# Performance work log

Measured on AMD Instinct MI355X. Metric: run time of the kernel, lower is better.

The kernel has to match this reference:

```python
import jax, jax.numpy as jnp
import numpy as np

B, C, H, W = 2, 256, 100, 100
G, P = 4, 8
CG = C // G  # 64 per-group channels
EPS = 1e-5


def setup_inputs() -> dict:
    key = jax.random.key(0)
    ks = jax.random.split(key, 5)
    bev_query = jax.random.normal(ks[0], (B, C, H, W), dtype=jnp.float32)
    pts = jax.random.normal(ks[1], (B, H * W, 1, P, C), dtype=jnp.float32)
    conv_w = jax.random.normal(ks[2], (G * CG * CG, C), dtype=jnp.float32) * (1.0 / np.sqrt(C))
    conv_b = jax.random.normal(ks[3], (G * CG * CG,), dtype=jnp.float32) * 0.02
    ln_g = jnp.ones((CG,), dtype=jnp.float32)
    ln_b = jnp.zeros((CG,), dtype=jnp.float32)
    proj_w = jax.random.normal(ks[4], (CG, CG * P), dtype=jnp.float32) * (1.0 / np.sqrt(CG * P))
    proj_b = jnp.zeros((CG,), dtype=jnp.float32)
    return {"bev_query": bev_query, "pts": pts, "conv_w": conv_w, "conv_b": conv_b,
            "ln_g": ln_g, "ln_b": ln_b, "proj_w": proj_w, "proj_b": proj_b}


def reference(bev_query, pts, conv_w, conv_b, ln_g, ln_b, proj_w, proj_b):
    b, c, h, w = bev_query.shape
    q = h * w
    # pts: b q 1 p c -> b q p c
    pts = jnp.squeeze(pts, axis=2)
    # 1x1 conv parameter generator: b c h w -> b (g c1 c2) h w
    param = jnp.einsum('bchw,oc->bohw', bev_query, conv_w) + conv_b[None, :, None, None]
    # 'b (g c1 c2) h w -> (b g) (h w) c1 c2'
    param = param.reshape(b, G, CG, CG, q).transpose(0, 1, 4, 2, 3).reshape(b * G, q, CG, CG)
    # 'b q p (g c) -> (b g) q p c'
    pts_g = pts.reshape(b, q, P, G, CG).transpose(0, 3, 1, 2, 4).reshape(b * G, q, P, CG)
    # batched per-pixel matmul: (bg,q,p,c1) @ (bg,q,c1,c2) -> (bg,q,p,c2)
    mixed = jnp.matmul(pts_g, param)
    # LayerNorm over last dim + ReLU
    mu = jnp.mean(mixed, axis=-1, keepdims=True)
    var = jnp.var(mixed, axis=-1, keepdims=True)
    normed = (mixed - mu) * jax.lax.rsqrt(var + EPS) * ln_g + ln_b
    act = jax.nn.relu(normed)
    # 'b q p c -> b q (p c)' then linear
    flat = act.reshape(b * G, q, P * CG)
    out = jnp.einsum('bqi,oi->bqo', flat, proj_w) + proj_b
    # '(b g) (h w) c -> b (g c) h w'
    out = out.reshape(b, G, q, CG).transpose(0, 1, 3, 2).reshape(b, G * CG, h, w)
    return out
```

## Files before the change

### kernel.cpp

```cpp
#include <hip/hip_runtime.h>
#include <hip/hip_bf16.h>
#include <stdint.h>

#define QTOT 10000
#define MPAD 10240
#define CDIM 256
#define ODIM 16384
#define RTOT 20096

using f32x4  = __attribute__((ext_vector_type(4))) float;
using bf16x8 = __attribute__((ext_vector_type(8))) short;

#define GLOAD_LDS(gp, lp) __builtin_amdgcn_global_load_lds(                     \
    (const __attribute__((address_space(1))) unsigned int*)(gp),                \
    (__attribute__((address_space(3))) unsigned int*)(lp), 16, 0, 0)

static __device__ __forceinline__ short f2bs(float x) {
  __hip_bfloat16 h = __float2bfloat16(x);
  return *(short*)&h;
}

__global__ void cvt_f32_bf16(const float* __restrict__ s, __hip_bfloat16* __restrict__ d, int n) {
  for (int i = blockIdx.x * blockDim.x + threadIdx.x; i < n; i += gridDim.x * blockDim.x)
    d[i] = __float2bfloat16(s[i]);
}

__global__ void cvt_permute_cw(const float* __restrict__ s, __hip_bfloat16* __restrict__ d, int n) {
  for (int i = blockIdx.x * blockDim.x + threadIdx.x; i < n; i += gridDim.x * blockDim.x) {
    int rn = i >> 8, c = i & 255;
    int ro = (rn & ~4095) | ((rn & 63) << 6) | ((rn >> 6) & 63);
    d[i] = __float2bfloat16(s[ro * 256 + c]);
  }
}

__global__ __launch_bounds__(256) void transpose_bev(const float* __restrict__ bev,
                                                     __hip_bfloat16* __restrict__ bevT) {
  __shared__ float tl[32][33];
  int tx = threadIdx.x, ty = threadIdx.y;
  int q0 = blockIdx.x * 32, c0 = blockIdx.y * 32, b = blockIdx.z;
#pragma unroll
  for (int i = 0; i < 4; ++i) {
    int c = c0 + ty + i * 8, q = q0 + tx;
    tl[ty + i * 8][tx] = (q < QTOT) ? bev[((size_t)b * CDIM + c) * QTOT + q] : 0.0f;
  }
  __syncthreads();
#pragma unroll
  for (int i = 0; i < 4; ++i) {
    int q = q0 + ty + i * 8, c = c0 + tx;
    bevT[((size_t)b * MPAD + q) * CDIM + c] = __float2bfloat16(tl[tx][ty + i * 8]);
  }
}

__global__ __launch_bounds__(256) void gemm_param(const __hip_bfloat16* __restrict__ A,
                                                  const __hip_bfloat16* __restrict__ Bw,
                                                  const float* __restrict__ convb,
                                                  __hip_bfloat16* __restrict__ P) {
  __shared__ __align__(16) unsigned char lsA[2][16384];
  __shared__ __align__(16) unsigned char lsB[2][16384];
  int t = threadIdx.x, lane = t & 63, w = t >> 6;
  int bm = blockIdx.x, bn = blockIdx.y;
  int wm = (w >> 1) * 64, wn = (w & 1) * 64;
  int srow = lane >> 3;
  int kbs  = ((lane & 7) ^ srow) * 8;
  const __hip_bfloat16* pA = A  + (size_t)(bm * 128 + w * 32 + srow) * CDIM + kbs;
  const __hip_bfloat16* pB = Bw + (size_t)(bn * 128 + w * 32 + srow) * CDIM + kbs;
  f32x4 acc[4][4] = {};

#define STAGE_P(buf, kt) do {                                                   \
    _Pragma("unroll")                                                           \
    for (int i = 0; i < 4; ++i) {                                               \
      GLOAD_LDS(pA + (size_t)i * 8 * CDIM + (kt), lsA[buf] + (w * 4 + i) * 1024); \
      GLOAD_LDS(pB + (size_t)i * 8 * CDIM + (kt), lsB[buf] + (w * 4 + i) * 1024); \
    } } while (0)

  STAGE_P(0, 0);
  asm volatile("s_waitcnt vmcnt(0)" ::: "memory");
  __builtin_amdgcn_s_barrier();
#pragma unroll
  for (int kt = 0; kt < 4; ++kt) {
    const int cur = kt & 1;
    if (kt < 3) STAGE_P(cur ^ 1, (kt + 1) * 64);
    __builtin_amdgcn_sched_barrier(0);
#pragma unroll
    for (int kk = 0; kk < 2; ++kk) {
      int kb = kk * 64 + ((lane >> 4) << 4);
      bf16x8 af[4], bfr[4];
#pragma unroll
      for (int mi = 0; mi < 4; ++mi) {
        int row = wm + mi * 16 + (lane & 15);
        af[mi] = *(const bf16x8*)(lsA[cur] + ((row * 128 + kb) ^ ((row & 7) << 4)));
      }
#pragma unroll
      for (int ni = 0; ni < 4; ++ni) {
        int row = wn + ni * 16 + (lane & 15);
        bfr[ni] = *(const bf16x8*)(lsB[cur] + ((row * 128 + kb) ^ ((row & 7) << 4)));
      }
#pragma unroll
      for (int mi = 0; mi < 4; ++mi)
#pragma unroll
        for (int ni = 0; ni < 4; ++ni)
          acc[mi][ni] = __builtin_amdgcn_mfma_f32_16x16x32_bf16(af[mi], bfr[ni], acc[mi][ni], 0, 0, 0);
    }
    __builtin_amdgcn_sched_barrier(0);
    if (kt < 3) asm volatile("s_waitcnt vmcnt(0)" ::: "memory");
    __builtin_amdgcn_s_barrier();
    __builtin_amdgcn_sched_barrier(0);
  }
#pragma unroll
  for (int ni = 0; ni < 4; ++ni) {
    int col = bn * 128 + wn + ni * 16 + (lane & 15);
    int o_old = (col & ~4095) | ((col & 63) << 6) | ((col >> 6) & 63);
    float cb = convb[o_old];
#pragma unroll
    for (int mi = 0; mi < 4; ++mi) {
      int rb = bm * 128 + wm + mi * 16 + ((lane >> 4) << 2);
#pragma unroll
      for (int r = 0; r < 4; ++r)
        P[(size_t)(rb + r) * ODIM + col] = __float2bfloat16(acc[mi][ni][r] + cb);
    }
  }
#undef STAGE_P
}

__global__ __launch_bounds__(256) void mix_mfma(const __hip_bfloat16* __restrict__ P,
                                                const float* __restrict__ pts,
                                                const float* __restrict__ lng,
                                                const float* __restrict__ lnb,
                                                __hip_bfloat16* __restrict__ act,
                                                int b, int q0) {
  __shared__ __align__(16) float ptsl[8 * 264];
  int t = threadIdx.x, lane = t & 63, g = t >> 6;
  int row = blockIdx.x;
  size_t rq = (size_t)b * QTOT + q0 + row;
  {
    const float4* ps = (const float4*)(pts + rq * 2048);
#pragma unroll
    for (int i = 0; i < 2; ++i) {
      int v = i * 256 + t;
      float4 val = ps[v];
      int p = v >> 6, c = (v & 63) * 4;
      *(float4*)(ptsl + p * 264 + c) = val;
    }
  }
  __syncthreads();
  int l15 = lane & 15, hi = lane >> 4;
  bf16x8 bfr[2];
#pragma unroll
  for (int kk = 0; kk < 2; ++kk) {
    bf16x8 v = {};
    if (l15 < 8) {
      const float* src = ptsl + l15 * 264 + g * 64 + kk * 32 + hi * 8;
#pragma unroll
      for (int j = 0; j < 8; ++j) v[j] = f2bs(src[j]);
    }
    bfr[kk] = v;
  }
  const __hip_bfloat16* Ap = P + (size_t)row * ODIM + g * 4096;
  f32x4 acc[4] = {};
#pragma unroll
  for (int kk = 0; kk < 2; ++kk)
#pragma unroll
    for (int mi = 0; mi < 4; ++mi) {
      bf16x8 a = *(const bf16x8*)(Ap + (size_t)(mi * 16 + l15) * 64 + kk * 32 + hi * 8);
      acc[mi] = __builtin_amdgcn_mfma_f32_16x16x32_bf16(a, bfr[kk], acc[mi], 0, 0, 0);
    }
  float s = 0.f, ss = 0.f;
#pragma unroll
  for (int mi = 0; mi < 4; ++mi)
#pragma unroll
    for (int r = 0; r < 4; ++r) { float v = acc[mi][r]; s += v; ss = fmaf(v, v, ss); }
  s += __shfl_xor(s, 16);  ss += __shfl_xor(ss, 16);
  s += __shfl_xor(s, 32);  ss += __shfl_xor(ss, 32);
  float mu  = s * 0.015625f;
  float var = ss * 0.015625f - mu * mu;
  float rs  = rsqrtf(var + 1e-5f);
  if (l15 < 8) {
    short* ab = (short*)act + ((size_t)g * RTOT + rq) * 512 + l15 * 64;
#pragma unroll
    for (int mi = 0; mi < 4; ++mi) {
      int c2 = mi * 16 + hi * 4;
      float4 gg = *(const float4*)(lng + c2);
      float4 bb = *(const float4*)(lnb + c2);
      short4 o;
      o.x = f2bs(fmaxf(0.f, (acc[mi][0] - mu) * rs * gg.x + bb.x));
      o.y = f2bs(fmaxf(0.f, (acc[mi][1] - mu) * rs * gg.y + bb.y));
      o.z = f2bs(fmaxf(0.f, (acc[mi][2] - mu) * rs * gg.z + bb.z));
      o.w = f2bs(fmaxf(0.f, (acc[mi][3] - mu) * rs * gg.w + bb.w));
      *(short4*)(ab + c2) = o;
    }
  }
}

__global__ __launch_bounds__(256) void gemm_proj(const __hip_bfloat16* __restrict__ act,
                                                 const __hip_bfloat16* __restrict__ Bp,
                                                 const float* __restrict__ projb,
                                                 float* __restrict__ outT) {
  __shared__ __align__(16) unsigned char lsA[2][16384];
  __shared__ __align__(16) unsigned char lsB[2][8192];
  int t = threadIdx.x, lane = t & 63, w = t >> 6;
  int bm = blockIdx.x, g = blockIdx.y;
  int wm = (w >> 1) * 64, wn = (w & 1) * 32;
  int srow = lane >> 3;
  int kbs  = ((lane & 7) ^ srow) * 8;
  const __hip_bfloat16* A  = act + (size_t)g * RTOT * 512;
  const __hip_bfloat16* pA = A  + (size_t)(bm * 128 + w * 32 + srow) * 512 + kbs;
  const __hip_bfloat16* pB = Bp + (size_t)(w * 16 + srow) * 512 + kbs;
  f32x4 acc[4][2] = {};

#define STAGE_Q(buf, kt) do {                                                   \
    _Pragma("unroll")                                                           \
    for (int i = 0; i < 4; ++i)                                                 \
      GLOAD_LDS(pA + (size_t)i * 8 * 512 + (kt), lsA[buf] + (w * 4 + i) * 1024); \
    _Pragma("unroll")                                                           \
    for (int j = 0; j < 2; ++j)                                                 \
      GLOAD_LDS(pB + (size_t)j * 8 * 512 + (kt), lsB[buf] + (w * 2 + j) * 1024); \
    } while (0)

  STAGE_Q(0, 0);
  asm volatile("s_waitcnt vmcnt(0)" ::: "memory");
  __builtin_amdgcn_s_barrier();
#pragma unroll
  for (int kt = 0; kt < 8; ++kt) {
    const int cur = kt & 1;
    if (kt < 7) STAGE_Q(cur ^ 1, (kt + 1) * 64);
    __builtin_amdgcn_sched_barrier(0);
#pragma unroll
    for (int kk = 0; kk < 2; ++kk) {
      int kb = kk * 64 + ((lane >> 4) << 4);
      bf16x8 af[4], bfr[2];
#pragma unroll
      for (int mi = 0; mi < 4; ++mi) {
        int row = wm + mi * 16 + (lane & 15);
        af[mi] = *(const bf16x8*)(lsA[cur] + ((row * 128 + kb) ^ ((row & 7) << 4)));
      }
#pragma unroll
      for (int ni = 0; ni < 2; ++ni) {
        int row = wn + ni * 16 + (lane & 15);
        bfr[ni] = *(const bf16x8*)(lsB[cur] + ((row * 128 + kb) ^ ((row & 7) << 4)));
      }
#pragma unroll
      for (int mi = 0; mi < 4; ++mi)
#pragma unroll
        for (int ni = 0; ni < 2; ++ni)
          acc[mi][ni] = __builtin_amdgcn_mfma_f32_16x16x32_bf16(af[mi], bfr[ni], acc[mi][ni], 0, 0, 0);
    }
    __builtin_amdgcn_sched_barrier(0);
    if (kt < 7) asm volatile("s_waitcnt vmcnt(0)" ::: "memory");
    __builtin_amdgcn_s_barrier();
    __builtin_amdgcn_sched_barrier(0);
  }
#pragma unroll
  for (int ni = 0; ni < 2; ++ni) {
    int o = wn + ni * 16 + (lane & 15);
    float pb = projb[o];
#pragma unroll
    for (int mi = 0; mi < 4; ++mi) {
      int rb = bm * 128 + wm + mi * 16 + ((lane >> 4) << 2);
#pragma unroll
      for (int r = 0; r < 4; ++r) {
        int rg = rb + r;
        if (rg < 2 * QTOT)
          outT[(size_t)rg * CDIM + g * 64 + o] = acc[mi][ni][r] + pb;
      }
    }
  }
#undef STAGE_Q
}

__global__ __launch_bounds__(256) void transpose_out(const float* __restrict__ outT,
                                                     float* __restrict__ out) {
  __shared__ float tl[32][33];
  int tx = threadIdx.x, ty = threadIdx.y;
  int q0 = blockIdx.x * 32, c0 = blockIdx.y * 32, b = blockIdx.z;
#pragma unroll
  for (int i = 0; i < 4; ++i) {
    int q = q0 + ty + i * 8, c = c0 + tx;
    tl[ty + i * 8][tx] = (q < QTOT) ? outT[((size_t)b * QTOT + q) * CDIM + c] : 0.0f;
  }
  __syncthreads();
#pragma unroll
  for (int i = 0; i < 4; ++i) {
    int c = c0 + ty + i * 8, q = q0 + tx;
    if (q < QTOT) out[((size_t)b * CDIM + c) * QTOT + q] = tl[tx][ty + i * 8];
  }
}

extern "C" void kernel_launch(void* const* d_in, const int* in_sizes, int n_in,
                              void* d_out, int out_size, void* d_ws, size_t ws_size,
                              hipStream_t stream) {
  const float* bev = (const float*)d_in[0];
  const float* pts = (const float*)d_in[1];
  const float* cw  = (const float*)d_in[2];
  const float* cb  = (const float*)d_in[3];
  const float* lng = (const float*)d_in[4];
  const float* lnb = (const float*)d_in[5];
  const float* pw  = (const float*)d_in[6];
  const float* pb  = (const float*)d_in[7];
  float* out = (float*)d_out;

  char* ws = (char*)d_ws;
  size_t off = 0;
  auto carve = [&](size_t bytes) -> char* {
    char* p = ws + off;
    off += (bytes + 255) & ~(size_t)255;
    return p;
  };
  __hip_bfloat16* cw_bf = (__hip_bfloat16*)carve((size_t)ODIM * CDIM * 2);
  __hip_bfloat16* bevT  = (__hip_bfloat16*)carve((size_t)2 * MPAD * CDIM * 2);
  __hip_bfloat16* pw_bf = (__hip_bfloat16*)carve((size_t)64 * 512 * 2);
  float* outT           = (float*)carve((size_t)2 * QTOT * CDIM * 4);
  __hip_bfloat16* act   = (__hip_bfloat16*)carve((size_t)4 * RTOT * 512 * 2);
  size_t fixed = off;

  int CH = 128;
  const int ladder[4] = {2560, 1280, 640, 128};
  for (int i = 0; i < 4; ++i) {
    size_t need = fixed + (((size_t)ladder[i] * ODIM * 2 + 255) & ~(size_t)255);
    if (need <= ws_size) { CH = ladder[i]; break; }
  }
  __hip_bfloat16* param = (__hip_bfloat16*)carve((size_t)CH * ODIM * 2);

  cvt_permute_cw<<<4096, 256, 0, stream>>>(cw, cw_bf, ODIM * CDIM);
  cvt_f32_bf16<<<128, 256, 0, stream>>>(pw, pw_bf, 64 * 512);
  transpose_bev<<<dim3(MPAD / 32, CDIM / 32, 2), dim3(32, 8), 0, stream>>>(bev, bevT);

  int nchunks = (QTOT + CH - 1) / CH;
  for (int b = 0; b < 2; ++b) {
    for (int c = 0; c < nchunks; ++c) {
      int q0 = c * CH;
      int nvalid = QTOT - q0;
      if (nvalid > CH) nvalid = CH;
      const __hip_bfloat16* Ab = bevT + ((size_t)b * MPAD + q0) * CDIM;
      gemm_param<<<dim3(CH / 128, ODIM / 128), 256, 0, stream>>>(Ab, cw_bf, cb, param);
      mix_mfma<<<dim3(nvalid), 256, 0, stream>>>(param, pts, lng, lnb, act, b, q0);
    }
  }
  gemm_proj<<<dim3(RTOT / 128, 4), 256, 0, stream>>>(act, pw_bf, pb, outT);
  transpose_out<<<dim3((QTOT + 31) / 32, CDIM / 32, 2), dim3(32, 8), 0, stream>>>(outT, out);
}
```

Baseline: 537.2 us.

## Enlarge param GEMM tile to 256x256 with 512 threads and block swizzle

Grows the parameter-generation GEMM block tile from 128x128 to 256x256, using 8 waves each computing a 128x64 sub-tile and doubling the LDS stage buffers. Block indices are remapped in groups of 8 to spread neighbouring tiles, which is meant to improve cache locality. The goal is more reuse of each staged A/B tile per global load. In mix_mfma the LDS staging of pts and the block barrier are replaced by direct float4 global loads. The chunk ladder drops the 1280/640 options, so small workspaces fall back to 256-row chunks. Risks are higher register and LDS pressure lowering occupancy, and fewer blocks per launch.

Measured after the change: 580.3 us. 8.0% more time.

```diff
diff --git a/kernel.cpp b/kernel.cpp
--- a/kernel.cpp
+++ b/kernel.cpp
@@ -51,20 +51,25 @@
   }
 }
 
-__global__ __launch_bounds__(256) void gemm_param(const __hip_bfloat16* __restrict__ A,
-                                                  const __hip_bfloat16* __restrict__ Bw,
-                                                  const float* __restrict__ convb,
-                                                  __hip_bfloat16* __restrict__ P) {
-  __shared__ __align__(16) unsigned char lsA[2][16384];
-  __shared__ __align__(16) unsigned char lsB[2][16384];
+__global__ __launch_bounds__(512, 2) void gemm_param(const __hip_bfloat16* __restrict__ A,
+                                                     const __hip_bfloat16* __restrict__ Bw,
+                                                     const float* __restrict__ convb,
+                                                     __hip_bfloat16* __restrict__ P,
+                                                     int nbm) {
+  __shared__ __align__(16) unsigned char lsA[2][32768];
+  __shared__ __align__(16) unsigned char lsB[2][32768];
   int t = threadIdx.x, lane = t & 63, w = t >> 6;
-  int bm = blockIdx.x, bn = blockIdx.y;
-  int wm = (w >> 1) * 64, wn = (w & 1) * 64;
+  int id = blockIdx.x + nbm * blockIdx.y;
+  int total = nbm * gridDim.y;
+  int nid = (total & 7) ? id : ((id & 7) * (total >> 3) + (id >> 3));
+  int bm = nid % nbm, bn = nid / nbm;
+  int wm = (w >> 2) * 128, wn = (w & 3) * 64;
+  int l15 = lane & 15, hi = lane >> 4;
   int srow = lane >> 3;
   int kbs  = ((lane & 7) ^ srow) * 8;
-  const __hip_bfloat16* pA = A  + (size_t)(bm * 128 + w * 32 + srow) * CDIM + kbs;
-  const __hip_bfloat16* pB = Bw + (size_t)(bn * 128 + w * 32 + srow) * CDIM + kbs;
-  f32x4 acc[4][4] = {};
+  const __hip_bfloat16* pA = A  + (size_t)(bm * 256 + w * 32 + srow) * CDIM + kbs;
+  const __hip_bfloat16* pB = Bw + (size_t)(bn * 256 + w * 32 + srow) * CDIM + kbs;
+  f32x4 acc[8][4] = {};
 
 #define STAGE_P(buf, kt) do {                                                   \
     _Pragma("unroll")                                                           \
@@ -83,20 +88,20 @@
     __builtin_amdgcn_sched_barrier(0);
 #pragma unroll
     for (int kk = 0; kk < 2; ++kk) {
-      int kb = kk * 64 + ((lane >> 4) << 4);
-      bf16x8 af[4], bfr[4];
-#pragma unroll
-      for (int mi = 0; mi < 4; ++mi) {
-        int row = wm + mi * 16 + (lane & 15);
+      int kb = kk * 64 + hi * 16;
+      bf16x8 af[8], bfr[4];
+#pragma unroll
+      for (int mi = 0; mi < 8; ++mi) {
+        int row = wm + mi * 16 + l15;
         af[mi] = *(const bf16x8*)(lsA[cur] + ((row * 128 + kb) ^ ((row & 7) << 4)));
       }
 #pragma unroll
       for (int ni = 0; ni < 4; ++ni) {
-        int row = wn + ni * 16 + (lane & 15);
+        int row = wn + ni * 16 + l15;
         bfr[ni] = *(const bf16x8*)(lsB[cur] + ((row * 128 + kb) ^ ((row & 7) << 4)));
       }
 #pragma unroll
-      for (int mi = 0; mi < 4; ++mi)
+      for (int mi = 0; mi < 8; ++mi)
 #pragma unroll
         for (int ni = 0; ni < 4; ++ni)
           acc[mi][ni] = __builtin_amdgcn_mfma_f32_16x16x32_bf16(af[mi], bfr[ni], acc[mi][ni], 0, 0, 0);
@@ -108,12 +113,12 @@
   }
 #pragma unroll
   for (int ni = 0; ni < 4; ++ni) {
-    int col = bn * 128 + wn + ni * 16 + (lane & 15);
+    int col = bn * 256 + wn + ni * 16 + l15;
     int o_old = (col & ~4095) | ((col & 63) << 6) | ((col >> 6) & 63);
     float cb = convb[o_old];
 #pragma unroll
-    for (int mi = 0; mi < 4; ++mi) {
-      int rb = bm * 128 + wm + mi * 16 + ((lane >> 4) << 2);
+    for (int mi = 0; mi < 8; ++mi) {
+      int rb = bm * 256 + wm + mi * 16 + hi * 4;
 #pragma unroll
       for (int r = 0; r < 4; ++r)
         P[(size_t)(rb + r) * ODIM + col] = __float2bfloat16(acc[mi][ni][r] + cb);
@@ -128,30 +133,20 @@
                                                 const float* __restrict__ lnb,
                                                 __hip_bfloat16* __restrict__ act,
                                                 int b, int q0) {
-  __shared__ __align__(16) float ptsl[8 * 264];
   int t = threadIdx.x, lane = t & 63, g = t >> 6;
   int row = blockIdx.x;
   size_t rq = (size_t)b * QTOT + q0 + row;
-  {
-    const float4* ps = (const float4*)(pts + rq * 2048);
-#pragma unroll
-    for (int i = 0; i < 2; ++i) {
-      int v = i * 256 + t;
-      float4 val = ps[v];
-      int p = v >> 6, c = (v & 63) * 4;
-      *(float4*)(ptsl + p * 264 + c) = val;
-    }
-  }
-  __syncthreads();
   int l15 = lane & 15, hi = lane >> 4;
+  const float* pp = pts + rq * 2048 + (size_t)l15 * 256 + g * 64 + hi * 8;
   bf16x8 bfr[2];
 #pragma unroll
   for (int kk = 0; kk < 2; ++kk) {
     bf16x8 v = {};
     if (l15 < 8) {
-      const float* src = ptsl + l15 * 264 + g * 64 + kk * 32 + hi * 8;
-#pragma unroll
-      for (int j = 0; j < 8; ++j) v[j] = f2bs(src[j]);
+      float4 f0 = *(const float4*)(pp + kk * 32);
+      float4 f1 = *(const float4*)(pp + kk * 32 + 4);
+      v[0] = f2bs(f0.x); v[1] = f2bs(f0.y); v[2] = f2bs(f0.z); v[3] = f2bs(f0.w);
+      v[4] = f2bs(f1.x); v[5] = f2bs(f1.y); v[6] = f2bs(f1.z); v[7] = f2bs(f1.w);
     }
     bfr[kk] = v;
   }
@@ -312,9 +307,9 @@
   __hip_bfloat16* act   = (__hip_bfloat16*)carve((size_t)4 * RTOT * 512 * 2);
   size_t fixed = off;
 
-  int CH = 128;
-  const int ladder[4] = {2560, 1280, 640, 128};
-  for (int i = 0; i < 4; ++i) {
+  int CH = 256;
+  const int ladder[2] = {2560, 256};
+  for (int i = 0; i < 2; ++i) {
     size_t need = fixed + (((size_t)ladder[i] * ODIM * 2 + 255) & ~(size_t)255);
     if (need <= ws_size) { CH = ladder[i]; break; }
   }
@@ -324,6 +319,7 @@
   cvt_f32_bf16<<<128, 256, 0, stream>>>(pw, pw_bf, 64 * 512);
   transpose_bev<<<dim3(MPAD / 32, CDIM / 32, 2), dim3(32, 8), 0, stream>>>(bev, bevT);
 
+  int nbm = CH / 256;
   int nchunks = (QTOT + CH - 1) / CH;
   for (int b = 0; b < 2; ++b) {
     for (int c = 0; c < nchunks; ++c) {
@@ -331,7 +327,7 @@
       int nvalid = QTOT - q0;
       if (nvalid > CH) nvalid = CH;
       const __hip_bfloat16* Ab = bevT + ((size_t)b * MPAD + q0) * CDIM;
-      gemm_param<<<dim3(CH / 128, ODIM / 128), 256, 0, stream>>>(Ab, cw_bf, cb, param);
+      gemm_param<<<dim3(nbm, ODIM / 256), 512, 0, stream>>>(Ab, cw_bf, cb, param, nbm);
       mix_mfma<<<dim3(nvalid), 256, 0, stream>>>(param, pts, lng, lnb, act, b, q0);
     }
   }
```

## Fuse projection GEMM and output transpose into mix kernel; remap gemm_param blocks

Applied to the files above, without the earlier changes.

The per-pixel mix kernel now handles 16 pixels per block. It stages the LayerNorm+ReLU activations in swizzled LDS and then runs the projection MFMA directly, writing the output in the final channel-major layout. This removes the global act buffer, the separate gemm_proj and transpose_out kernels, and the outT round trip. gemm_param also gets a block-id remap that interleaves blocks across groups of 8, likely to spread work across XCDs. The cost is a serial 16-pixel loop with a barrier per pixel and 64KB of LDS per block, which can lower occupancy.

After: 777.3 us. 1.45x slower.

```diff
diff --git a/kernel.cpp b/kernel.cpp
--- a/kernel.cpp
+++ b/kernel.cpp
@@ -6,7 +6,6 @@
 #define MPAD 10240
 #define CDIM 256
 #define ODIM 16384
-#define RTOT 20096
 
 using f32x4  = __attribute__((ext_vector_type(4))) float;
 using bf16x8 = __attribute__((ext_vector_type(8))) short;
@@ -54,11 +53,15 @@
 __global__ __launch_bounds__(256) void gemm_param(const __hip_bfloat16* __restrict__ A,
                                                   const __hip_bfloat16* __restrict__ Bw,
                                                   const float* __restrict__ convb,
-                                                  __hip_bfloat16* __restrict__ P) {
+                                                  __hip_bfloat16* __restrict__ P,
+                                                  int nbm) {
   __shared__ __align__(16) unsigned char lsA[2][16384];
   __shared__ __align__(16) unsigned char lsB[2][16384];
   int t = threadIdx.x, lane = t & 63, w = t >> 6;
-  int bm = blockIdx.x, bn = blockIdx.y;
+  int id = blockIdx.x + nbm * blockIdx.y;
+  int total = nbm * gridDim.y;
+  int nid = (total & 7) ? id : ((id & 7) * (total >> 3) + (id >> 3));
+  int bm = nid % nbm, bn = nid / nbm;
   int wm = (w >> 1) * 64, wn = (w & 1) * 64;
   int srow = lane >> 3;
   int kbs  = ((lane & 7) ^ srow) * 8;
@@ -122,17 +125,30 @@
 #undef STAGE_P
 }
 
-__global__ __launch_bounds__(256) void mix_mfma(const __hip_bfloat16* __restrict__ P,
-                                                const float* __restrict__ pts,
-                                                const float* __restrict__ lng,
-                                                const float* __restrict__ lnb,
-                                                __hip_bfloat16* __restrict__ act,
-                                                int b, int q0) {
+__global__ __launch_bounds__(256) void mix_fused(const __hip_bfloat16* __restrict__ P,
+                                                 const float* __restrict__ pts,
+                                                 const float* __restrict__ lng,
+                                                 const float* __restrict__ lnb,
+                                                 const __hip_bfloat16* __restrict__ pw,
+                                                 const float* __restrict__ pb,
+                                                 float* __restrict__ out,
+                                                 int b, int q0, int nvalid) {
   __shared__ __align__(16) float ptsl[8 * 264];
+  __shared__ __align__(16) unsigned char actl[16 * 4096];
   int t = threadIdx.x, lane = t & 63, g = t >> 6;
-  int row = blockIdx.x;
-  size_t rq = (size_t)b * QTOT + q0 + row;
-  {
+  int l15 = lane & 15, hi = lane >> 4;
+  int rowbase = blockIdx.x * 16;
+  float gg[4][4], bbv[4][4];
+#pragma unroll
+  for (int mi = 0; mi < 4; ++mi) {
+    int c2 = mi * 16 + hi * 4;
+    *(float4*)gg[mi]  = *(const float4*)(lng + c2);
+    *(float4*)bbv[mi] = *(const float4*)(lnb + c2);
+  }
+  for (int px = 0; px < 16; ++px) {
+    int rcl = rowbase + px;
+    if (rcl >= nvalid) rcl = nvalid - 1;
+    size_t rq = (size_t)b * QTOT + q0 + rcl;
     const float4* ps = (const float4*)(pts + rq * 2048);
 #pragma unroll
     for (int i = 0; i < 2; ++i) {
@@ -141,147 +157,81 @@
       int p = v >> 6, c = (v & 63) * 4;
       *(float4*)(ptsl + p * 264 + c) = val;
     }
-  }
-  __syncthreads();
-  int l15 = lane & 15, hi = lane >> 4;
-  bf16x8 bfr[2];
-#pragma unroll
-  for (int kk = 0; kk < 2; ++kk) {
-    bf16x8 v = {};
+    __syncthreads();
+    bf16x8 bfr[2];
+#pragma unroll
+    for (int kk = 0; kk < 2; ++kk) {
+      bf16x8 v = {};
+      if (l15 < 8) {
+        const float* src = ptsl + l15 * 264 + g * 64 + kk * 32 + hi * 8;
+#pragma unroll
+        for (int j = 0; j < 8; ++j) v[j] = f2bs(src[j]);
+      }
+      bfr[kk] = v;
+    }
+    const __hip_bfloat16* Ap = P + (size_t)rcl * ODIM + g * 4096;
+    f32x4 acc[4] = {};
+#pragma unroll
+    for (int kk = 0; kk < 2; ++kk)
+#pragma unroll
+      for (int mi = 0; mi < 4; ++mi) {
+        bf16x8 a = *(const bf16x8*)(Ap + (size_t)(mi * 16 + l15) * 64 + kk * 32 + hi * 8);
+        acc[mi] = __builtin_amdgcn_mfma_f32_16x16x32_bf16(a, bfr[kk], acc[mi], 0, 0, 0);
+      }
+    float s = 0.f, ss = 0.f;
+#pragma unroll
+    for (int mi = 0; mi < 4; ++mi)
+#pragma unroll
+      for (int r = 0; r < 4; ++r) { float v = acc[mi][r]; s += v; ss = fmaf(v, v, ss); }
+    s += __shfl_xor(s, 16);  ss += __shfl_xor(ss, 16);
+    s += __shfl_xor(s, 32);  ss += __shfl_xor(ss, 32);
+    float mu  = s * 0.015625f;
+    float var = ss * 0.015625f - mu * mu;
+    float rs  = rsqrtf(var + 1e-5f);
     if (l15 < 8) {
-      const float* src = ptsl + l15 * 264 + g * 64 + kk * 32 + hi * 8;
-#pragma unroll
-      for (int j = 0; j < 8; ++j) v[j] = f2bs(src[j]);
-    }
-    bfr[kk] = v;
-  }
-  const __hip_bfloat16* Ap = P + (size_t)row * ODIM + g * 4096;
-  f32x4 acc[4] = {};
-#pragma unroll
-  for (int kk = 0; kk < 2; ++kk)
-#pragma unroll
-    for (int mi = 0; mi < 4; ++mi) {
-      bf16x8 a = *(const bf16x8*)(Ap + (size_t)(mi * 16 + l15) * 64 + kk * 32 + hi * 8);
-      acc[mi] = __builtin_amdgcn_mfma_f32_16x16x32_bf16(a, bfr[kk], acc[mi], 0, 0, 0);
-    }
-  float s = 0.f, ss = 0.f;
-#pragma unroll
-  for (int mi = 0; mi < 4; ++mi)
-#pragma unroll
-    for (int r = 0; r < 4; ++r) { float v = acc[mi][r]; s += v; ss = fmaf(v, v, ss); }
-  s += __shfl_xor(s, 16);  ss += __shfl_xor(ss, 16);
-  s += __shfl_xor(s, 32);  ss += __shfl_xor(ss, 32);
-  float mu  = s * 0.015625f;
-  float var = ss * 0.015625f - mu * mu;
-  float rs  = rsqrtf(var + 1e-5f);
-  if (l15 < 8) {
-    short* ab = (short*)act + ((size_t)g * RTOT + rq) * 512 + l15 * 64;
-#pragma unroll
-    for (int mi = 0; mi < 4; ++mi) {
-      int c2 = mi * 16 + hi * 4;
-      float4 gg = *(const float4*)(lng + c2);
-      float4 bb = *(const float4*)(lnb + c2);
-      short4 o;
-      o.x = f2bs(fmaxf(0.f, (acc[mi][0] - mu) * rs * gg.x + bb.x));
-      o.y = f2bs(fmaxf(0.f, (acc[mi][1] - mu) * rs * gg.y + bb.y));
-      o.z = f2bs(fmaxf(0.f, (acc[mi][2] - mu) * rs * gg.z + bb.z));
-      o.w = f2bs(fmaxf(0.f, (acc[mi][3] - mu) * rs * gg.w + bb.w));
-      *(short4*)(ab + c2) = o;
-    }
-  }
-}
-
-__global__ __launch_bounds__(256) void gemm_proj(const __hip_bfloat16* __restrict__ act,
-                                                 const __hip_bfloat16* __restrict__ Bp,
-                                                 const float* __restrict__ projb,
-                                                 float* __restrict__ outT) {
-  __shared__ __align__(16) unsigned char lsA[2][16384];
-  __shared__ __align__(16) unsigned char lsB[2][8192];
-  int t = threadIdx.x, lane = t & 63, w = t >> 6;
-  int bm = blockIdx.x, g = blockIdx.y;
-  int wm = (w >> 1) * 64, wn = (w & 1) * 32;
-  int srow = lane >> 3;
-  int kbs  = ((lane & 7) ^ srow) * 8;
-  const __hip_bfloat16* A  = act + (size_t)g * RTOT * 512;
-  const __hip_bfloat16* pA = A  + (size_t)(bm * 128 + w * 32 + srow) * 512 + kbs;
-  const __hip_bfloat16* pB = Bp + (size_t)(w * 16 + srow) * 512 + kbs;
-  f32x4 acc[4][2] = {};
-
-#define STAGE_Q(buf, kt) do {                                                   \
-    _Pragma("unroll")                                                           \
-    for (int i = 0; i < 4; ++i)                                                 \
-      GLOAD_LDS(pA + (size_t)i * 8 * 512 + (kt), lsA[buf] + (w * 4 + i) * 1024); \
-    _Pragma("unroll")                                                           \
-    for (int j = 0; j < 2; ++j)                                                 \
-      GLOAD_LDS(pB + (size_t)j * 8 * 512 + (kt), lsB[buf] + (w * 2 + j) * 1024); \
-    } while (0)
-
-  STAGE_Q(0, 0);
-  asm volatile("s_waitcnt vmcnt(0)" ::: "memory");
-  __builtin_amdgcn_s_barrier();
-#pragma unroll
-  for (int kt = 0; kt < 8; ++kt) {
-    const int cur = kt & 1;
-    if (kt < 7) STAGE_Q(cur ^ 1, (kt + 1) * 64);
-    __builtin_amdgcn_sched_barrier(0);
-#pragma unroll
-    for (int kk = 0; kk < 2; ++kk) {
-      int kb = kk * 64 + ((lane >> 4) << 4);
-      bf16x8 af[4], bfr[2];
+      int base = px * 4096 + g * 1024 + l15 * 128;
 #pragma unroll
       for (int mi = 0; mi < 4; ++mi) {
-        int row = wm + mi * 16 + (lane & 15);
-        af[mi] = *(const bf16x8*)(lsA[cur] + ((row * 128 + kb) ^ ((row & 7) << 4)));
-      }
-#pragma unroll
-      for (int ni = 0; ni < 2; ++ni) {
-        int row = wn + ni * 16 + (lane & 15);
-        bfr[ni] = *(const bf16x8*)(lsB[cur] + ((row * 128 + kb) ^ ((row & 7) << 4)));
-      }
-#pragma unroll
-      for (int mi = 0; mi < 4; ++mi)
-#pragma unroll
-        for (int ni = 0; ni < 2; ++ni)
-          acc[mi][ni] = __builtin_amdgcn_mfma_f32_16x16x32_bf16(af[mi], bfr[ni], acc[mi][ni], 0, 0, 0);
-    }
-    __builtin_amdgcn_sched_barrier(0);
-    if (kt < 7) asm volatile("s_waitcnt vmcnt(0)" ::: "memory");
-    __builtin_amdgcn_s_barrier();
-    __builtin_amdgcn_sched_barrier(0);
-  }
-#pragma unroll
-  for (int ni = 0; ni < 2; ++ni) {
-    int o = wn + ni * 16 + (lane & 15);
-    float pb = projb[o];
-#pragma unroll
-    for (int mi = 0; mi < 4; ++mi) {
-      int rb = bm * 128 + wm + mi * 16 + ((lane >> 4) << 2);
-#pragma unroll
-      for (int r = 0; r < 4; ++r) {
-        int rg = rb + r;
-        if (rg < 2 * QTOT)
-          outT[(size_t)rg * CDIM + g * 64 + o] = acc[mi][ni][r] + pb;
-      }
-    }
-  }
-#undef STAGE_Q
-}
-
-__global__ __launch_bounds__(256) void transpose_out(const float* __restrict__ outT,
-                                                     float* __restrict__ out) {
-  __shared__ float tl[32][33];
-  int tx = threadIdx.x, ty = threadIdx.y;
-  int q0 = blockIdx.x * 32, c0 = blockIdx.y * 32, b = blockIdx.z;
-#pragma unroll
-  for (int i = 0; i < 4; ++i) {
-    int q = q0 + ty + i * 8, c = c0 + tx;
-    tl[ty + i * 8][tx] = (q < QTOT) ? outT[((size_t)b * QTOT + q) * CDIM + c] : 0.0f;
-  }
-  __syncthreads();
-#pragma unroll
-  for (int i = 0; i < 4; ++i) {
-    int c = c0 + ty + i * 8, q = q0 + tx;
-    if (q < QTOT) out[((size_t)b * CDIM + c) * QTOT + q] = tl[tx][ty + i * 8];
+        short4 o;
+        o.x = f2bs(fmaxf(0.f, (acc[mi][0] - mu) * rs * gg[mi][0] + bbv[mi][0]));
+        o.y = f2bs(fmaxf(0.f, (acc[mi][1] - mu) * rs * gg[mi][1] + bbv[mi][1]));
+        o.z = f2bs(fmaxf(0.f, (acc[mi][2] - mu) * rs * gg[mi][2] + bbv[mi][2]));
+        o.w = f2bs(fmaxf(0.f, (acc[mi][3] - mu) * rs * gg[mi][3] + bbv[mi][3]));
+        int addr = (base + (mi * 16 + hi * 4) * 2) ^ ((px & 7) << 4);
+        *(short4*)(actl + addr) = o;
+      }
+    }
+    __syncthreads();
+  }
+  f32x4 pacc[4] = {};
+  const __hip_bfloat16* Bg = pw;
+#pragma unroll
+  for (int kk = 0; kk < 16; ++kk) {
+    int addr = (l15 * 4096 + g * 1024 + kk * 64 + hi * 16) ^ ((l15 & 7) << 4);
+    bf16x8 af = *(const bf16x8*)(actl + addr);
+#pragma unroll
+    for (int ni = 0; ni < 4; ++ni) {
+      bf16x8 bf = *(const bf16x8*)(Bg + (size_t)(ni * 16 + l15) * 512 + kk * 32 + hi * 8);
+      pacc[ni] = __builtin_amdgcn_mfma_f32_16x16x32_bf16(af, bf, pacc[ni], 0, 0, 0);
+    }
+  }
+#pragma unroll
+  for (int ni = 0; ni < 4; ++ni) {
+    int c2o = ni * 16 + l15;
+    int c = g * 64 + c2o;
+    float pbv = pb[c2o];
+    int qv = q0 + rowbase + hi * 4;
+    float* op = out + ((size_t)b * CDIM + c) * QTOT + qv;
+    if (qv + 3 < QTOT) {
+      float4 o4;
+      o4.x = pacc[ni][0] + pbv; o4.y = pacc[ni][1] + pbv;
+      o4.z = pacc[ni][2] + pbv; o4.w = pacc[ni][3] + pbv;
+      *(float4*)op = o4;
+    } else {
+#pragma unroll
+      for (int r = 0; r < 4; ++r)
+        if (qv + r < QTOT) op[r] = pacc[ni][r] + pbv;
+    }
   }
 }
 
@@ -308,8 +258,6 @@
   __hip_bfloat16* cw_bf = (__hip_bfloat16*)carve((size_t)ODIM * CDIM * 2);
   __hip_bfloat16* bevT  = (__hip_bfloat16*)carve((size_t)2 * MPAD * CDIM * 2);
   __hip_bfloat16* pw_bf = (__hip_bfloat16*)carve((size_t)64 * 512 * 2);
-  float* outT           = (float*)carve((size_t)2 * QTOT * CDIM * 4);
-  __hip_bfloat16* act   = (__hip_bfloat16*)carve((size_t)4 * RTOT * 512 * 2);
   size_t fixed = off;
 
   int CH = 128;
@@ -324,6 +272,7 @@
   cvt_f32_bf16<<<128, 256, 0, stream>>>(pw, pw_bf, 64 * 512);
   transpose_bev<<<dim3(MPAD / 32, CDIM / 32, 2), dim3(32, 8), 0, stream>>>(bev, bevT);
 
+  int nbm = CH / 128;
   int nchunks = (QTOT + CH - 1) / CH;
   for (int b = 0; b < 2; ++b) {
     for (int c = 0; c < nchunks; ++c) {
@@ -331,10 +280,9 @@
       int nvalid = QTOT - q0;
       if (nvalid > CH) nvalid = CH;
       const __hip_bfloat16* Ab = bevT + ((size_t)b * MPAD + q0) * CDIM;
-      gemm_param<<<dim3(CH / 128, ODIM / 128), 256, 0, stream>>>(Ab, cw_bf, cb, param);
-      mix_mfma<<<dim3(nvalid), 256, 0, stream>>>(param, pts, lng, lnb, act, b, q0);
-    }
-  }
-  gemm_proj<<<dim3(RTOT / 128, 4), 256, 0, stream>>>(act, pw_bf, pb, outT);
-  transpose_out<<<dim3((QTOT + 31) / 32, CDIM / 32, 2), dim3(32, 8), 0, stream>>>(outT, out);
-}
+      gemm_param<<<dim3(nbm, ODIM / 128), 256, 0, stream>>>(Ab, cw_bf, cb, param, nbm);
+      mix_fused<<<dim3((nvalid + 15) / 16), 256, 0, stream>>>(param, pts, lng, lnb,
+                                                              pw_bf, pb, out, b, q0, nvalid);
+    }
+  }
+}
```
